# Kernel optimization log

Hardware: AMD Instinct MI355X
Metric: run time of the kernel (lower is better)

Reference implementation:

```python
import jax, jax.numpy as jnp
import numpy as np

BATCH, SEQ_LEN, INPUT_DIM, HIDDEN, OUT_DIM = 4096, 2048, 5, 64, 1
DT = 0.1


def setup_inputs() -> dict:
    key = jax.random.key(0)
    ks = jax.random.split(key, 8)
    return {
        "x": jax.random.normal(ks[0], (BATCH, SEQ_LEN, INPUT_DIM), dtype=jnp.float32),
        # torch.rand(hidden)*0.5 + 0.1  -> uniform in [0.1, 0.6)
        "time_constants": jax.random.uniform(ks[1], (HIDDEN,), dtype=jnp.float32) * 0.5 + 0.1,
        "W_ih_w": jax.random.normal(ks[2], (HIDDEN, INPUT_DIM), dtype=jnp.float32) * (1.0 / np.sqrt(INPUT_DIM)),
        "W_ih_b": jax.random.normal(ks[3], (HIDDEN,), dtype=jnp.float32) * 0.02,
        "W_hh_w": jax.random.normal(ks[4], (HIDDEN, HIDDEN), dtype=jnp.float32) * (1.0 / np.sqrt(HIDDEN)),
        "W_hh_b": jax.random.normal(ks[5], (HIDDEN,), dtype=jnp.float32) * 0.02,
        "out_w": jax.random.normal(ks[6], (OUT_DIM, HIDDEN), dtype=jnp.float32) * (1.0 / np.sqrt(HIDDEN)),
        "out_b": jax.random.normal(ks[7], (OUT_DIM,), dtype=jnp.float32) * 0.02,
    }


def reference(x, time_constants, W_ih_w, W_ih_b, W_hh_w, W_hh_b, out_w, out_b):
    # x: [B, T, D_in]. Liquid-time-constant RNN: sequential scan over T.
    batch = x.shape[0]
    hidden = time_constants.shape[0]
    inv_tau = 1.0 / jnp.abs(time_constants)  # [H], hoisted out of the loop

    def step(h, x_t):
        # x_t: [B, D_in], h: [B, H]
        input_current = x_t @ W_ih_w.T + W_ih_b            # [B, H]
        recurrent_current = jnp.tanh(h) @ W_hh_w.T + W_hh_b  # [B, H]
        dhdt = -h * inv_tau + input_current + recurrent_current
        return h + DT * dhdt, None

    h0 = jnp.zeros((batch, hidden), dtype=x.dtype)
    xs = jnp.swapaxes(x, 0, 1)  # [T, B, D_in]
    h_final, _ = jax.lax.scan(step, h0, xs)
    return jnp.tanh(h_final) @ out_w.T + out_b  # [B, out_dim]
```

## Files before the change

kernel.cpp:

```cpp
#include <hip/hip_runtime.h>
#include <hip/hip_bf16.h>
#include <stdint.h>

#define SEQ   2048
#define DIN   5
#define HID   64
#define DTC   0.1f
#define BTILE 16
#define NWAVE 4

typedef __attribute__((ext_vector_type(8))) __bf16  bf16x8;
typedef __attribute__((ext_vector_type(8))) short   short8;
typedef __attribute__((ext_vector_type(4))) float   f32x4;
typedef __attribute__((ext_vector_type(4))) int     i32x4;
typedef __attribute__((ext_vector_type(2))) int     i32x2;
typedef unsigned long long u64;

__device__ __forceinline__ unsigned short f2bf(float f) {
    unsigned int u = __builtin_bit_cast(unsigned int, f);
    return (unsigned short)((u + 0x7FFFu + ((u >> 16) & 1u)) >> 16);
}

__device__ __forceinline__ float fast_tanh(float x) {
    float e = __expf(2.0f * x);
    return 1.0f - 2.0f * __builtin_amdgcn_rcpf(e + 1.0f);
}

__device__ __forceinline__ unsigned int cvt_pk_bf16(float lo, float hi) {
    unsigned int r;
    asm("v_cvt_pk_bf16_f32 %0, %1, %2" : "=v"(r) : "v"(lo), "v"(hi));
    return r;
}

__global__ __launch_bounds__(256) void ltc_kernel(
    const float* __restrict__ x,
    const float* __restrict__ tau,
    const float* __restrict__ Wih,
    const float* __restrict__ bih,
    const float* __restrict__ Whh,
    const float* __restrict__ bhh,
    const float* __restrict__ outw,
    const float* __restrict__ outb,
    float* __restrict__ out)
{
    const int tid  = threadIdx.x;
    const int wave = tid >> 6;
    const int lane = tid & 63;
    const int lg   = lane >> 4;
    const int ln   = lane & 15;
    const int b0   = blockIdx.x * BTILE;

    __shared__ __align__(16) unsigned short sbuf[2][1024];
    __shared__ float redbuf[NWAVE][4][BTILE];

    const int jbase = 16 * wave + 4 * lg;
    const int arow  = 16 * wave + ln;

    float a[4], ow[4];
#pragma unroll
    for (int r = 0; r < 4; ++r) {
        a[r]  = 1.0f - DTC / fabsf(tau[jbase + r]);
        ow[r] = outw[jbase + r];
    }

    short8 s0 = {0,0,0,0,0,0,0,0}, s1 = {0,0,0,0,0,0,0,0}, s2 = {0,0,0,0,0,0,0,0};
#pragma unroll
    for (int q = 0; q < 8; ++q) {
        s0[q] = (short)f2bf(DTC * Whh[arow * HID + lg * 8 + q]);
        s1[q] = (short)f2bf(DTC * Whh[arow * HID + 32 + lg * 8 + q]);
    }
    if (lg == 0) {
#pragma unroll
        for (int d = 0; d < DIN; ++d) s2[d] = (short)f2bf(DTC * Wih[arow * DIN + d]);
        s2[5] = (short)f2bf(DTC * (bih[arow] + bhh[arow]));
    }
    const bf16x8 Ahh0 = __builtin_bit_cast(bf16x8, s0);
    const bf16x8 Ahh1 = __builtin_bit_cast(bf16x8, s1);
    const bf16x8 Aix  = __builtin_bit_cast(bf16x8, s2);

    const int wbyte = ((jbase >= 32) ? 1024 : 0) + (((jbase & 31) >> 3) * 256)
                    + ln * 16 + (((jbase >> 2) & 1) * 8);
    char* const wp0 = (char*)sbuf[0] + wbyte;
    char* const wp1 = (char*)sbuf[1] + wbyte;
    const char* const rp0 = (const char*)sbuf[0] + lane * 16;
    const char* const rp1 = (const char*)sbuf[1] + lane * 16;

    ((u64*)sbuf[1])[tid] = 0ULL;

    const float* xb = x + (size_t)(b0 + ln) * (SEQ * DIN);
    f32x4 bufA[10], bufB[10];
#pragma unroll
    for (int i = 0; i < 10; ++i) bufA[i] = *(const f32x4*)(xb + 4 * i);

    f32x4 h = {0.f, 0.f, 0.f, 0.f};

#define SBAR() asm volatile("s_waitcnt lgkmcnt(0)\n\ts_barrier" ::: "memory")

#define BODY(PAR, X0, X1, X2, X3, X4)                                              \
    {                                                                              \
        const char* rb = (PAR) ? rp0 : rp1;                \
        i32x4 r0 = *(const i32x4*)(rb);                                            \
        i32x4 r1 = *(const i32x4*)(rb + 1024);                                     \
        i32x4 bx;                                                                  \
        bx[0] = (int)cvt_pk_bf16(X0, X1);                                          \
        bx[1] = (int)cvt_pk_bf16(X2, X3);                                          \
        bx[2] = (int)cvt_pk_bf16(X4, 1.0f);                                        \
        bx[3] = 0;                                                                 \
        f32x4 c;                                                                   \
        c[0] = a[0]*h[0]; c[1] = a[1]*h[1]; c[2] = a[2]*h[2]; c[3] = a[3]*h[3];    \
        c = __builtin_amdgcn_mfma_f32_16x16x32_bf16(Aix,  __builtin_bit_cast(bf16x8, bx), c, 0, 0, 0); \
        c = __builtin_amdgcn_mfma_f32_16x16x32_bf16(Ahh0, __builtin_bit_cast(bf16x8, r0), c, 0, 0, 0); \
        c = __builtin_amdgcn_mfma_f32_16x16x32_bf16(Ahh1, __builtin_bit_cast(bf16x8, r1), c, 0, 0, 0); \
        h = c;                                                                     \
        float t0 = fast_tanh(c[0]), t1 = fast_tanh(c[1]);                          \
        float t2 = fast_tanh(c[2]), t3 = fast_tanh(c[3]);                          \
        i32x2 w; w[0] = (int)cvt_pk_bf16(t0, t1); w[1] = (int)cvt_pk_bf16(t2, t3); \
        *(i32x2*)((PAR) ? wp1 : wp0) = w;                                          \
    }

#define SUPER(BUF, DO_LOAD, LBUF, LOFF)                                            \
    SBAR();                                                                        \
    if (DO_LOAD) {                                                                 \
        _Pragma("unroll")                                                          \
        for (int i = 0; i < 10; ++i) LBUF[i] = *(const f32x4*)(xb + (LOFF) + 4*i); \
    }                                                                              \
    BODY(0, BUF[0][0], BUF[0][1], BUF[0][2], BUF[0][3], BUF[1][0])                 \
    SBAR(); BODY(1, BUF[1][1], BUF[1][2], BUF[1][3], BUF[2][0], BUF[2][1])         \
    SBAR(); BODY(0, BUF[2][2], BUF[2][3], BUF[3][0], BUF[3][1], BUF[3][2])         \
    SBAR(); BODY(1, BUF[3][3], BUF[4][0], BUF[4][1], BUF[4][2], BUF[4][3])         \
    SBAR(); BODY(0, BUF[5][0], BUF[5][1], BUF[5][2], BUF[5][3], BUF[6][0])         \
    SBAR(); BODY(1, BUF[6][1], BUF[6][2], BUF[6][3], BUF[7][0], BUF[7][1])         \
    SBAR(); BODY(0, BUF[7][2], BUF[7][3], BUF[8][0], BUF[8][1], BUF[8][2])         \
    SBAR(); BODY(1, BUF[8][3], BUF[9][0], BUF[9][1], BUF[9][2], BUF[9][3])

    for (int it = 0; it < SEQ / 16; ++it) {
        SUPER(bufA, true,            bufB, (it * 16 + 8)  * DIN)
        SUPER(bufB, it != SEQ/16 - 1, bufA, (it * 16 + 16) * DIN)
    }
#undef SUPER
#undef BODY
#undef SBAR

    float part = fast_tanh(h[0]) * ow[0] + fast_tanh(h[1]) * ow[1]
               + fast_tanh(h[2]) * ow[2] + fast_tanh(h[3]) * ow[3];
    redbuf[wave][lg][ln] = part;
    __syncthreads();
    if (tid < BTILE) {
        float s = outb[0];
#pragma unroll
        for (int w = 0; w < NWAVE; ++w)
#pragma unroll
            for (int g = 0; g < 4; ++g) s += redbuf[w][g][tid];
        out[b0 + tid] = s;
    }
}

extern "C" void kernel_launch(void* const* d_in, const int* in_sizes, int n_in,
                              void* d_out, int out_size, void* d_ws, size_t ws_size,
                              hipStream_t stream) {
    const float* x    = (const float*)d_in[0];
    const float* tau  = (const float*)d_in[1];
    const float* Wih  = (const float*)d_in[2];
    const float* bih  = (const float*)d_in[3];
    const float* Whh  = (const float*)d_in[4];
    const float* bhh  = (const float*)d_in[5];
    const float* outw = (const float*)d_in[6];
    const float* outb = (const float*)d_in[7];
    float* out = (float*)d_out;

    const int batch = in_sizes[0] / (SEQ * DIN);
    ltc_kernel<<<batch / BTILE, NWAVE * 64, 0, stream>>>(x, tau, Wih, bih, Whh, bhh, outw, outb, out);
}
```

Before: 531.7 us.

## Halve waves per block and give each wave two interleaved hidden-row MFMA tiles

```diff
diff --git a/kernel.cpp b/kernel.cpp
--- a/kernel.cpp
+++ b/kernel.cpp
@@ -7,7 +7,7 @@
 #define HID   64
 #define DTC   0.1f
 #define BTILE 16
-#define NWAVE 4
+#define NWAVE 2
 
 typedef __attribute__((ext_vector_type(8))) __bf16  bf16x8;
 typedef __attribute__((ext_vector_type(8))) short   short8;
@@ -32,7 +32,7 @@
     return r;
 }
 
-__global__ __launch_bounds__(256) void ltc_kernel(
+__global__ __launch_bounds__(128) void ltc_kernel(
     const float* __restrict__ x,
     const float* __restrict__ tau,
     const float* __restrict__ Wih,
@@ -53,46 +53,51 @@
     __shared__ __align__(16) unsigned short sbuf[2][1024];
     __shared__ float redbuf[NWAVE][4][BTILE];
 
-    const int jbase = 16 * wave + 4 * lg;
-    const int arow  = 16 * wave + ln;
-
-    float a[4], ow[4];
+    float a[2][4], ow[2][4];
+    bf16x8 Ahh[2][2], Aix[2];
+    int wbyte[2];
 #pragma unroll
-    for (int r = 0; r < 4; ++r) {
-        a[r]  = 1.0f - DTC / fabsf(tau[jbase + r]);
-        ow[r] = outw[jbase + r];
+    for (int m = 0; m < 2; ++m) {
+        const int jb   = 32 * wave + 16 * m + 4 * lg;
+        const int arow = 32 * wave + 16 * m + ln;
+#pragma unroll
+        for (int r = 0; r < 4; ++r) {
+            a[m][r]  = 1.0f - DTC / fabsf(tau[jb + r]);
+            ow[m][r] = outw[jb + r];
+        }
+#pragma unroll
+        for (int kt = 0; kt < 2; ++kt) {
+            short8 s;
+#pragma unroll
+            for (int q = 0; q < 8; ++q)
+                s[q] = (short)f2bf(DTC * Whh[arow * HID + kt * 32 + lg * 8 + q]);
+            Ahh[m][kt] = __builtin_bit_cast(bf16x8, s);
+        }
+        short8 sx = {0,0,0,0,0,0,0,0};
+        if (lg == 0) {
+#pragma unroll
+            for (int d = 0; d < DIN; ++d) sx[d] = (short)f2bf(DTC * Wih[arow * DIN + d]);
+            sx[5] = (short)f2bf(DTC * (bih[arow] + bhh[arow]));
+        }
+        Aix[m] = __builtin_bit_cast(bf16x8, sx);
+        wbyte[m] = ((jb >= 32) ? 1024 : 0) + (((jb & 31) >> 3) * 256)
+                 + ln * 16 + (((jb >> 2) & 1) * 8);
     }
 
-    short8 s0 = {0,0,0,0,0,0,0,0}, s1 = {0,0,0,0,0,0,0,0}, s2 = {0,0,0,0,0,0,0,0};
-#pragma unroll
-    for (int q = 0; q < 8; ++q) {
-        s0[q] = (short)f2bf(DTC * Whh[arow * HID + lg * 8 + q]);
-        s1[q] = (short)f2bf(DTC * Whh[arow * HID + 32 + lg * 8 + q]);
-    }
-    if (lg == 0) {
-#pragma unroll
-        for (int d = 0; d < DIN; ++d) s2[d] = (short)f2bf(DTC * Wih[arow * DIN + d]);
-        s2[5] = (short)f2bf(DTC * (bih[arow] + bhh[arow]));
-    }
-    const bf16x8 Ahh0 = __builtin_bit_cast(bf16x8, s0);
-    const bf16x8 Ahh1 = __builtin_bit_cast(bf16x8, s1);
-    const bf16x8 Aix  = __builtin_bit_cast(bf16x8, s2);
-
-    const int wbyte = ((jbase >= 32) ? 1024 : 0) + (((jbase & 31) >> 3) * 256)
-                    + ln * 16 + (((jbase >> 2) & 1) * 8);
-    char* const wp0 = (char*)sbuf[0] + wbyte;
-    char* const wp1 = (char*)sbuf[1] + wbyte;
     const char* const rp0 = (const char*)sbuf[0] + lane * 16;
     const char* const rp1 = (const char*)sbuf[1] + lane * 16;
 
-    ((u64*)sbuf[1])[tid] = 0ULL;
+    ((u64*)sbuf[1])[tid]       = 0ULL;
+    ((u64*)sbuf[1])[tid + 128] = 0ULL;
 
     const float* xb = x + (size_t)(b0 + ln) * (SEQ * DIN);
     f32x4 bufA[10], bufB[10];
 #pragma unroll
     for (int i = 0; i < 10; ++i) bufA[i] = *(const f32x4*)(xb + 4 * i);
 
-    f32x4 h = {0.f, 0.f, 0.f, 0.f};
+    f32x4 h[2];
+#pragma unroll
+    for (int m = 0; m < 2; ++m) { h[m][0]=0.f; h[m][1]=0.f; h[m][2]=0.f; h[m][3]=0.f; }
 
 #define SBAR() asm volatile("s_waitcnt lgkmcnt(0)\n\ts_barrier" ::: "memory")
 
@@ -106,16 +111,27 @@
         bx[1] = (int)cvt_pk_bf16(X2, X3);                                          \
         bx[2] = (int)cvt_pk_bf16(X4, 1.0f);                                        \
         bx[3] = 0;                                                                 \
-        f32x4 c;                                                                   \
-        c[0] = a[0]*h[0]; c[1] = a[1]*h[1]; c[2] = a[2]*h[2]; c[3] = a[3]*h[3];    \
-        c = __builtin_amdgcn_mfma_f32_16x16x32_bf16(Aix,  __builtin_bit_cast(bf16x8, bx), c, 0, 0, 0); \
-        c = __builtin_amdgcn_mfma_f32_16x16x32_bf16(Ahh0, __builtin_bit_cast(bf16x8, r0), c, 0, 0, 0); \
-        c = __builtin_amdgcn_mfma_f32_16x16x32_bf16(Ahh1, __builtin_bit_cast(bf16x8, r1), c, 0, 0, 0); \
-        h = c;                                                                     \
-        float t0 = fast_tanh(c[0]), t1 = fast_tanh(c[1]);                          \
-        float t2 = fast_tanh(c[2]), t3 = fast_tanh(c[3]);                          \
-        i32x2 w; w[0] = (int)cvt_pk_bf16(t0, t1); w[1] = (int)cvt_pk_bf16(t2, t3); \
-        *(i32x2*)((PAR) ? wp1 : wp0) = w;                                          \
+        f32x4 c0, c1;                                                              \
+        c0[0] = a[0][0]*h[0][0]; c0[1] = a[0][1]*h[0][1];                          \
+        c0[2] = a[0][2]*h[0][2]; c0[3] = a[0][3]*h[0][3];                          \
+        c1[0] = a[1][0]*h[1][0]; c1[1] = a[1][1]*h[1][1];                          \
+        c1[2] = a[1][2]*h[1][2]; c1[3] = a[1][3]*h[1][3];                          \
+        c0 = __builtin_amdgcn_mfma_f32_16x16x32_bf16(Aix[0], __builtin_bit_cast(bf16x8, bx), c0, 0, 0, 0); \
+        c1 = __builtin_amdgcn_mfma_f32_16x16x32_bf16(Aix[1], __builtin_bit_cast(bf16x8, bx), c1, 0, 0, 0); \
+        c0 = __builtin_amdgcn_mfma_f32_16x16x32_bf16(Ahh[0][0], __builtin_bit_cast(bf16x8, r0), c0, 0, 0, 0); \
+        c1 = __builtin_amdgcn_mfma_f32_16x16x32_bf16(Ahh[1][0], __builtin_bit_cast(bf16x8, r0), c1, 0, 0, 0); \
+        c0 = __builtin_amdgcn_mfma_f32_16x16x32_bf16(Ahh[0][1], __builtin_bit_cast(bf16x8, r1), c0, 0, 0, 0); \
+        c1 = __builtin_amdgcn_mfma_f32_16x16x32_bf16(Ahh[1][1], __builtin_bit_cast(bf16x8, r1), c1, 0, 0, 0); \
+        h[0] = c0; h[1] = c1;                                                      \
+        float t00 = fast_tanh(c0[0]), t01 = fast_tanh(c0[1]);                      \
+        float t02 = fast_tanh(c0[2]), t03 = fast_tanh(c0[3]);                      \
+        float t10 = fast_tanh(c1[0]), t11 = fast_tanh(c1[1]);                      \
+        float t12 = fast_tanh(c1[2]), t13 = fast_tanh(c1[3]);                      \
+        char* wb = (char*)sbuf[(PAR)];                                             \
+        i32x2 w0; w0[0] = (int)cvt_pk_bf16(t00, t01); w0[1] = (int)cvt_pk_bf16(t02, t03); \
+        i32x2 w1; w1[0] = (int)cvt_pk_bf16(t10, t11); w1[1] = (int)cvt_pk_bf16(t12, t13); \
+        *(i32x2*)(wb + wbyte[0]) = w0;                                             \
+        *(i32x2*)(wb + wbyte[1]) = w1;                                             \
     }
 
 #define SUPER(BUF, DO_LOAD, LBUF, LOFF)                                            \
@@ -141,8 +157,12 @@
 #undef BODY
 #undef SBAR
 
-    float part = fast_tanh(h[0]) * ow[0] + fast_tanh(h[1]) * ow[1]
-               + fast_tanh(h[2]) * ow[2] + fast_tanh(h[3]) * ow[3];
+    float part = 0.0f;
+#pragma unroll
+    for (int m = 0; m < 2; ++m)
+#pragma unroll
+        for (int r = 0; r < 4; ++r)
+            part += fast_tanh(h[m][r]) * ow[m][r];
     redbuf[wave][lg][ln] = part;
     __syncthreads();
     if (tid < BTILE) {
```

Result: slower. 631.9 us (+18.8%).
